# Kernel optimization log

Hardware: AMD Instinct MI355X
Metric: run time of the kernel (lower is better)

The kernel has to match this reference:

```python
import jax, jax.numpy as jnp
import numpy as np

B, S, HID = 1, 2048, 4096
NH, NKV = 32, 8
HD = HID // NH            # 128
GROUPS = NH // NKV        # 4
ROPE_THETA = 10000.0


def _rope_cos_sin(seq_len, head_dim, dtype=jnp.float32):
    inv_freq = 1.0 / (ROPE_THETA ** (jnp.arange(0, head_dim, 2, dtype=jnp.float32) / head_dim))
    t = jnp.arange(seq_len, dtype=jnp.float32)
    freqs = jnp.outer(t, inv_freq)                      # [S, HD/2]
    emb = jnp.concatenate([freqs, freqs], axis=-1)      # [S, HD]
    return jnp.cos(emb).astype(dtype), jnp.sin(emb).astype(dtype)


def _rotate_half(x):
    x1, x2 = jnp.split(x, 2, axis=-1)
    return jnp.concatenate([-x2, x1], axis=-1)


def _apply_rope(x, cos, sin):
    # x: [B, H, S, HD]; cos/sin: [S, HD] (position_ids = arange(S), no past)
    return x * cos[None, None] + _rotate_half(x) * sin[None, None]


def setup_inputs() -> dict:
    key = jax.random.key(0)
    k1, k2, k3, k4, k5 = jax.random.split(key, 5)
    return {
        "hidden_states": jax.random.normal(k1, (B, S, HID), jnp.float32),
        "Wq": jax.random.normal(k2, (NH * HD, HID), jnp.float32) * 0.02,
        "Wk": jax.random.normal(k3, (NKV * HD, HID), jnp.float32) * 0.02,
        "Wv": jax.random.normal(k4, (NKV * HD, HID), jnp.float32) * 0.02,
        "Wo": jax.random.normal(k5, (HID, NH * HD), jnp.float32) * 0.02,
    }


def reference(hidden_states, Wq, Wk, Wv, Wo):
    bsz, q_len, _ = hidden_states.shape
    # projections (nn.Linear: x @ W.T)
    q = (hidden_states @ Wq.T).reshape(bsz, q_len, NH, HD).transpose(0, 2, 1, 3)   # [B,NH,S,HD]
    k = (hidden_states @ Wk.T).reshape(bsz, q_len, NKV, HD).transpose(0, 2, 1, 3)  # [B,NKV,S,HD]
    v = (hidden_states @ Wv.T).reshape(bsz, q_len, NKV, HD).transpose(0, 2, 1, 3)

    cos, sin = _rope_cos_sin(q_len, HD, hidden_states.dtype)
    q = _apply_rope(q, cos, sin)
    k = _apply_rope(k, cos, sin)

    # GQA: repeat kv heads (repeat_kv / num_key_value_groups)
    k = jnp.repeat(k, GROUPS, axis=1)   # [B,NH,S,HD]
    v = jnp.repeat(v, GROUPS, axis=1)

    scale = 1.0 / jnp.sqrt(jnp.asarray(HD, hidden_states.dtype))
    logits = jnp.einsum('bhqd,bhkd->bhqk', q, k) * scale   # [B,NH,S,S]

    # prefill causal mask (phys_past_len = 0)
    causal = jnp.tril(jnp.ones((q_len, q_len), dtype=bool))
    logits = jnp.where(causal[None, None], logits, jnp.finfo(logits.dtype).min)

    attn = jax.nn.softmax(logits, axis=-1)
    out = jnp.einsum('bhqk,bhkd->bhqd', attn, v)            # [B,NH,S,HD]
    out = out.transpose(0, 2, 1, 3).reshape(bsz, q_len, NH * HD)
    return out @ Wo.T
```

## Files before the change

### kernel.cpp

```cpp
#include <hip/hip_runtime.h>

typedef __bf16 bf16;
typedef __bf16 bf16x2 __attribute__((ext_vector_type(2)));
typedef __bf16 bf16x4 __attribute__((ext_vector_type(4)));
typedef __bf16 bf16x8 __attribute__((ext_vector_type(8)));
typedef float f32x4 __attribute__((ext_vector_type(4)));

#define S_LEN 2048
#define HID_DIM 4096
#define NH 32
#define NKV 8
#define HD 128
#define QKV_N 6144
#define K_COL 4096
#define V_COL 5120
#define PADV 76

__global__ void cvt_all_kernel(const float* __restrict__ hs, const float* __restrict__ wq,
                               const float* __restrict__ wk, const float* __restrict__ wv,
                               const float* __restrict__ wo, bf16* __restrict__ hsb,
                               bf16* __restrict__ wqkvb, bf16* __restrict__ wob,
                               float* __restrict__ cost, float* __restrict__ sint) {
  long i = (long)blockIdx.x * blockDim.x + threadIdx.x;
  if (i >= 12582912) {
    int j = (int)(i - 12582912);
    int s = j >> 6, d = j & 63;
    float inv = expf(-0.14391156831212787f * (float)d);
    float ang = (float)s * inv;
    cost[j] = cosf(ang);
    sint[j] = sinf(ang);
    return;
  }
  const float* src; bf16* dst; long off; bool perm = false;
  if (i < 2097152)      { src = hs; dst = hsb;                          off = i; }
  else if (i < 6291456) { src = wq; dst = wqkvb;                        off = i - 2097152; perm = true; }
  else if (i < 7340032) { src = wk; dst = wqkvb + (long)4096 * 4096;    off = i - 6291456; perm = true; }
  else if (i < 8388608) { src = wv; dst = wqkvb + (long)5120 * 4096;    off = i - 7340032; }
  else                  { src = wo; dst = wob;                          off = i - 8388608; }
  float4 v = reinterpret_cast<const float4*>(src)[off];
  bf16x4 o;
  o[0] = (bf16)v.x; o[1] = (bf16)v.y; o[2] = (bf16)v.z; o[3] = (bf16)v.w;
  long doff = off;
  if (perm) {
    long r = off >> 10, c4 = off & 1023;
    long d = r & 127;
    long pd = ((d & 63) << 1) | (d >> 6);
    doff = (((r & ~127L) | pd) << 10) | c4;
  }
  reinterpret_cast<bf16x4*>(dst)[doff] = o;
}

#define STG8(buf, mat, kt, unit) {                                                       \
    const bf16* sp_ = (mat) ? Bp : Ap;                                                   \
    int row0_ = ((mat) ? n0 : m0) + (unit) * 64;                                         \
    int lb_ = (buf) * LBUF + (mat) * 16384 + (unit) * 4096;                              \
    int r_ = t >> 3, jl_ = t & 7, jg_ = jl_ ^ (r_ & 7);                                  \
    const bf16* src_ = sp_ + (long)(row0_ + r_) * K + (kt) * 64 + jg_ * 8;               \
    __builtin_amdgcn_global_load_lds((const __attribute__((address_space(1))) void*)src_,\
        (__attribute__((address_space(3))) void*)(L + lb_ + t * 8), 16, 0, 0); }

#define DSA2(buf, mh) {                                                                  \
    _Pragma("unroll") for (int ks_ = 0; ks_ < 2; ++ks_)                                  \
      _Pragma("unroll") for (int mf_ = 0; mf_ < 4; ++mf_) {                              \
        int R_ = wr * 128 + (mh) * 64 + mf_ * 16 + lm;                                   \
        aF[ks_][mf_] = *reinterpret_cast<const bf16x8*>(                                 \
            L + (buf) * LBUF + R_ * 64 + (((ks_ * 4 + lg) ^ (R_ & 7)) << 3));            \
      } }

#define DSBALL(buf) {                                                                    \
    _Pragma("unroll") for (int ks_ = 0; ks_ < 2; ++ks_)                                  \
      _Pragma("unroll") for (int nf_ = 0; nf_ < NB; ++nf_) {                             \
        int R_ = wc * (NB * 16) + nf_ * 16 + lm;                                         \
        bF[ks_][nf_] = *reinterpret_cast<const bf16x8*>(                                 \
            L + (buf) * LBUF + 16384 + R_ * 64 + (((ks_ * 4 + lg) ^ (R_ & 7)) << 3));    \
      } }

#define MM2(mh) {                                                                        \
    __builtin_amdgcn_s_setprio(1);                                                       \
    _Pragma("unroll") for (int mf_ = 0; mf_ < 4; ++mf_)                                  \
      _Pragma("unroll") for (int nf_ = 0; nf_ < NB; ++nf_)                               \
        _Pragma("unroll") for (int ks_ = 0; ks_ < 2; ++ks_)                              \
          acc[(mh) * 4 + mf_][nf_] = __builtin_amdgcn_mfma_f32_16x16x32_bf16(            \
              aF[ks_][mf_], bF[ks_][nf_], acc[(mh) * 4 + mf_][nf_], 0, 0, 0);            \
    __builtin_amdgcn_s_setprio(0); }

#define BAR() __builtin_amdgcn_s_barrier()
#define WVM(n) asm volatile("s_waitcnt vmcnt(%0)" :: "i"(n) : "memory")

template<int NB, bool ROPE, typename OutT>
__global__ __launch_bounds__(512, 1) void gemm4p_kernel(
    const bf16* __restrict__ Ap, const bf16* __restrict__ Bp, OutT* __restrict__ C,
    int M, int N, int K, const float* __restrict__ cost, const float* __restrict__ sint) {
  constexpr int LBUF = 16384 + NB * 4096;
  __shared__ __align__(16) bf16 L[2 * LBUF];

  int nwg = gridDim.x * gridDim.y;
  int bid = blockIdx.y * gridDim.x + blockIdx.x;
  int cpx = nwg >> 3;
  int swz = (bid & 7) * cpx + (bid >> 3);
  int bxs = swz % gridDim.x, bys = swz / gridDim.x;
  const int n0 = bxs * (NB * 64), m0 = bys * 256;

  const int t = threadIdx.x;
  const int lane = t & 63, w = t >> 6;
  const int wr = w >> 2, wc = w & 3;
  const int lg = lane >> 4, lm = lane & 15;
  const int NT = K >> 6;

  f32x4 acc[8][NB] = {};
  bf16x8 aF[2][4], bF[2][NB];

  STG8(0, 0, 0, 0); STG8(0, 0, 0, 1); STG8(0, 0, 0, 2); STG8(0, 0, 0, 3);
  STG8(0, 1, 0, 0); if (NB > 1) STG8(0, 1, 0, 1); if (NB > 2) STG8(0, 1, 0, 2);
  STG8(1, 1, 1, 0); if (NB > 1) STG8(1, 1, 1, 1); if (NB > 2) STG8(1, 1, 1, 2);
  WVM(NB);
  BAR();

  for (int I = 0; I < (NT >> 1); ++I) {
    const int tt = 2 * I;
    const bool pf = (I < (NT >> 1) - 1);
    DSA2(0, 0); DSBALL(0);
    STG8(1, 0, tt + 1, 0); STG8(1, 0, tt + 1, 1);
    STG8(1, 0, tt + 1, 2); STG8(1, 0, tt + 1, 3);
    BAR(); MM2(0); BAR();
    DSA2(0, 1);
    if (pf) { STG8(0, 1, tt + 2, 0); if (NB > 1) STG8(0, 1, tt + 2, 1);
              if (NB > 2) STG8(0, 1, tt + 2, 2); }
    BAR(); MM2(1);
    if (pf) WVM(NB); else WVM(0);
    BAR();
    DSA2(1, 0); DSBALL(1);
    if (pf) { STG8(0, 0, tt + 2, 0); STG8(0, 0, tt + 2, 1);
              STG8(0, 0, tt + 2, 2); STG8(0, 0, tt + 2, 3); }
    BAR(); MM2(0); BAR();
    DSA2(1, 1);
    if (pf) { STG8(1, 1, tt + 3, 0); if (NB > 1) STG8(1, 1, tt + 3, 1);
              if (NB > 2) STG8(1, 1, tt + 3, 2); }
    BAR(); MM2(1);
    if (pf) WVM(NB); else WVM(0);
    BAR();
  }

#pragma unroll
  for (int am = 0; am < 8; ++am) {
    int row = m0 + wr * 128 + am * 16 + lg * 4;
#pragma unroll
    for (int nf = 0; nf < NB; ++nf) {
      int col = n0 + wc * (NB * 16) + nf * 16 + lm;
      if (ROPE && col < V_COL) {
        int j = (col & 127) >> 1;
        bool odd = col & 1;
#pragma unroll
        for (int rr = 0; rr < 4; ++rr) {
          float x = acc[am][nf][rr];
          float xp = __shfl_xor(x, 1);
          int s = row + rr;
          float cv = cost[(s << 6) | j], sv = sint[(s << 6) | j];
          float y = odd ? (x * cv + xp * sv) : (x * cv - xp * sv);
          C[(long)s * N + col] = (bf16)y;
        }
      } else {
#pragma unroll
        for (int rr = 0; rr < 4; ++rr) {
          float v = acc[am][nf][rr];
          if constexpr (sizeof(OutT) == 4) C[(long)(row + rr) * N + col] = v;
          else                             C[(long)(row + rr) * N + col] = (bf16)v;
        }
      }
    }
  }
}

#define AK_BAR() { asm volatile("s_waitcnt vmcnt(2)" ::: "memory");                      \
                   __builtin_amdgcn_sched_barrier(0);                                    \
                   asm volatile("s_waitcnt lgkmcnt(0)" ::: "memory");                    \
                   __builtin_amdgcn_s_barrier(); }

#define AK_WRITEV(r0, r1, vtb) {                                                         \
    _Pragma("unroll") for (int e = 0; e < 8; ++e) {                                      \
      bf16x2 pk; pk[0] = r0[e]; pk[1] = r1[e];                                           \
      *reinterpret_cast<bf16x2*>(Vt[vtb] + (dchunk * 8 + e) * PADV + slot) = pk;         \
    } }

#define AK_ISSUEV(base, r0, r1) {                                                        \
    long rv_ = (long)(base) + kva; if (rv_ > 2046) rv_ = 2046;                           \
    const bf16* vs_ = vbase + rv_ * QKV_N + dchunk * 8;                                  \
    r0 = *reinterpret_cast<const bf16x8*>(vs_);                                          \
    r1 = *reinterpret_cast<const bf16x8*>(vs_ + QKV_N); }

#define AK_ISSUEK(base, buf) {                                                           \
    _Pragma("unroll") for (int i_ = 0; i_ < 2; ++i_) {                                   \
      int c_ = i_ * 512 + t;                                                             \
      int r_ = c_ >> 4, jl_ = c_ & 15, jg_ = jl_ ^ (r_ & 15);                            \
      long rk_ = (long)(base) + r_; if (rk_ > 2047) rk_ = 2047;                          \
      const bf16* src_ = kbase + rk_ * QKV_N + jg_ * 8;                                  \
      __builtin_amdgcn_global_load_lds((const __attribute__((address_space(1))) void*)src_,\
          (__attribute__((address_space(3))) void*)(Ks[buf] + c_ * 8), 16, 0, 0);        \
    } }

#define AK_STEP(stv, bufb) {                                                             \
    const int st_ = (stv);                                                               \
    const int kv0_ = st_ * 64;                                                           \
    if (kv0_ <= q0 + w * 16 + 15) {                                                      \
      f32x4 s[4];                                                                        \
      _Pragma("unroll") for (int cb = 0; cb < 4; ++cb) s[cb] = f32x4{0.f,0.f,0.f,0.f};   \
      __builtin_amdgcn_s_setprio(1);                                                     \
      _Pragma("unroll") for (int ks = 0; ks < 4; ++ks)                                   \
        _Pragma("unroll") for (int cb = 0; cb < 4; ++cb) {                               \
          bf16x8 kf = *reinterpret_cast<const bf16x8*>(                                  \
              Ks[bufb] + (cb * 16 + lm) * 128 + (((ks * 4 + lg) ^ lm) << 3));            \
          s[cb] = __builtin_amdgcn_mfma_f32_16x16x32_bf16(kf, qf[ks], s[cb], 0, 0, 0);   \
        }                                                                                \
      __builtin_amdgcn_s_setprio(0);                                                     \
      const float SC = 0.12751742f;                                                      \
      float sl[4][4];                                                                    \
      _Pragma("unroll") for (int cb = 0; cb < 4; ++cb)                                   \
        _Pragma("unroll") for (int r = 0; r < 4; ++r) {                                  \
          float v = s[cb][r] * SC;                                                       \
          if (st_ >= nst - 2 && (kv0_ + cb * 16 + lg * 4 + r) > qg) v = -1e30f;          \
          sl[cb][r] = v;                                                                 \
        }                                                                                \
      float tm = sl[0][0];                                                               \
      _Pragma("unroll") for (int cb = 0; cb < 4; ++cb)                                   \
        _Pragma("unroll") for (int r = 0; r < 4; ++r) tm = fmaxf(tm, sl[cb][r]);         \
      tm = fmaxf(tm, __shfl_xor(tm, 16));                                                \
      tm = fmaxf(tm, __shfl_xor(tm, 32));                                                \
      if (__any(tm > mrow + 8.f)) {                                                      \
        float mnew = fmaxf(mrow, tm);                                                    \
        float alpha = exp2f(mrow - mnew);                                                \
        mrow = mnew; lrow *= alpha;                                                      \
        float ar[4];                                                                     \
        _Pragma("unroll") for (int r = 0; r < 4; ++r)                                    \
          ar[r] = __shfl(alpha, (lane & 48) | (lg * 4 + r));                             \
        _Pragma("unroll") for (int i = 0; i < 8; ++i)                                    \
          _Pragma("unroll") for (int r = 0; r < 4; ++r) o[i][r] *= ar[r];                \
      }                                                                                  \
      float p[4][4]; float psum = 0.f;                                                   \
      _Pragma("unroll") for (int cb = 0; cb < 4; ++cb)                                   \
        _Pragma("unroll") for (int r = 0; r < 4; ++r) {                                  \
          p[cb][r] = exp2f(sl[cb][r] - mrow); psum += p[cb][r];                          \
        }                                                                                \
      psum += __shfl_xor(psum, 16);                                                      \
      psum += __shfl_xor(psum, 32);                                                      \
      lrow += psum;                                                                      \
      bf16x8 pa0, pa1;                                                                   \
      _Pragma("unroll") for (int r = 0; r < 4; ++r) {                                    \
        pa0[r] = (bf16)p[0][r]; pa0[4 + r] = (bf16)p[1][r];                              \
        pa1[r] = (bf16)p[2][r]; pa1[4 + r] = (bf16)p[3][r];                              \
      }                                                                                  \
      __builtin_amdgcn_s_setprio(1);                                                     \
      _Pragma("unroll") for (int db = 0; db < 8; ++db) {                                 \
        bf16x8 vf0 = *reinterpret_cast<const bf16x8*>(Vt[bufb] + (db*16+lm)*PADV + lg*8);\
        bf16x8 vf1 = *reinterpret_cast<const bf16x8*>(Vt[bufb] + (db*16+lm)*PADV + 32 + lg*8);\
        o[db] = __builtin_amdgcn_mfma_f32_16x16x32_bf16(pa0, vf0, o[db], 0, 0, 0);       \
        o[db] = __builtin_amdgcn_mfma_f32_16x16x32_bf16(pa1, vf1, o[db], 0, 0, 0);       \
      }                                                                                  \
      __builtin_amdgcn_s_setprio(0);                                                     \
    } }

__global__ __launch_bounds__(512, 4) void attn_kernel(const bf16* __restrict__ qkv,
                                                      bf16* __restrict__ out) {
  __shared__ __align__(16) bf16 Ks[2][64 * 128];
  __shared__ __align__(16) bf16 Vt[2][128 * PADV];

  const int bx = blockIdx.x;
  const int qt = (bx < 256) ? (15 - (bx >> 5)) : ((bx - 256) >> 5);
  const int h = bx & 31;
  const int kvh = h >> 2;
  const int q0 = qt * 128;
  const int t = threadIdx.x, lane = t & 63, w = t >> 6;
  const int lg = lane >> 4, lm = lane & 15;
  const int dchunk = t >> 5, kv2 = t & 31;
  const int kva = kv2 * 2;
  const int k5 = kva & 31;
  const int slot = ((kva >> 5) << 5) | (((k5 >> 2) & 3) << 3) | ((k5 >> 4) << 2) | (k5 & 3);
  const bf16* kbase = qkv + K_COL + kvh * HD;
  const bf16* vbase = qkv + V_COL + kvh * HD;

  const long qrow = q0 + w * 16 + lm;
  const int qg = q0 + w * 16 + lm;
  bf16x8 qf[4];
#pragma unroll
  for (int ks = 0; ks < 4; ++ks)
    qf[ks] = *reinterpret_cast<const bf16x8*>(qkv + qrow * QKV_N + h * HD + ks * 32 + lg * 8);

  f32x4 o[8];
#pragma unroll
  for (int i = 0; i < 8; ++i) o[i] = f32x4{0.f, 0.f, 0.f, 0.f};
  float mrow = -1e30f, lrow = 0.f;

  const int nst = 2 * qt + 2;
  bf16x8 va0, va1, vb0, vb1;

  AK_ISSUEK(0, 0);
  AK_ISSUEV(0, va0, va1);
  AK_WRITEV(va0, va1, 0);
  AK_ISSUEV(64, vb0, vb1);
  asm volatile("s_waitcnt lgkmcnt(0)" ::: "memory");
  __builtin_amdgcn_s_barrier();

  for (int I = 0; I < (nst >> 1); ++I) {
    const int s0 = 2 * I;
    AK_ISSUEK((s0 + 1) * 64, 1);
    AK_ISSUEV((s0 + 2) * 64, va0, va1);
    AK_WRITEV(vb0, vb1, 1);
    AK_STEP(s0, 0);
    AK_BAR();
    AK_ISSUEK((s0 + 2) * 64, 0);
    AK_ISSUEV((s0 + 3) * 64, vb0, vb1);
    AK_WRITEV(va0, va1, 0);
    AK_STEP(s0 + 1, 1);
    AK_BAR();
  }

  float invr[4];
#pragma unroll
  for (int r = 0; r < 4; ++r)
    invr[r] = 1.0f / __shfl(lrow, (lane & 48) | (lg * 4 + r));
#pragma unroll
  for (int r = 0; r < 4; ++r) {
    long row = q0 + w * 16 + lg * 4 + r;
#pragma unroll
    for (int db = 0; db < 8; ++db)
      out[row * HID_DIM + h * HD + db * 16 + lm] = (bf16)(o[db][r] * invr[r]);
  }
}

extern "C" void kernel_launch(void* const* d_in, const int* in_sizes, int n_in,
                              void* d_out, int out_size, void* d_ws, size_t ws_size,
                              hipStream_t stream) {
  const float* hs = (const float*)d_in[0];
  const float* Wq = (const float*)d_in[1];
  const float* Wk = (const float*)d_in[2];
  const float* Wv = (const float*)d_in[3];
  const float* Wo = (const float*)d_in[4];
  float* out = (float*)d_out;
  char* ws = (char*)d_ws;

  bf16*  hsb   = (bf16*)(ws);
  bf16*  wqkvb = (bf16*)(ws + 16777216);
  bf16*  wob   = (bf16*)(ws + 67108864);
  bf16*  qkv   = (bf16*)(ws + 100663296);
  bf16*  attn  = (bf16*)(ws + 125829120);
  float* cost  = (float*)(ws + 142606336);
  float* sint  = (float*)(ws + 143130624);

  cvt_all_kernel<<<49664, 256, 0, stream>>>(hs, Wq, Wk, Wv, Wo, hsb, wqkvb, wob, cost, sint);
  gemm4p_kernel<3, true, bf16><<<dim3(32, 8), 512, 0, stream>>>(hsb, wqkvb, qkv, 2048, 6144, 4096, cost, sint);
  attn_kernel<<<512, 512, 0, stream>>>(qkv, attn);
  gemm4p_kernel<2, false, float><<<dim3(32, 8), 512, 0, stream>>>(attn, wob, out, 2048, 4096, 4096, nullptr, nullptr);
}
```

Measured before the change: 297.5 us.

## Rework attention kernel to 32x32x16 MFMA with 4 waves of 32 query rows

The attention kernel switches from 16x16x32 MFMA tiles with 8 waves of 16 query rows to 32x32x16 MFMA tiles with 4 waves of 32 query rows each (256 threads per block). K/V staging loads are widened per thread to cover the tile with half the threads, and the Vt swizzle and softmax row-shuffle indexing are rewritten for the 32x32 accumulator layout. Separately, RoPE cos/sin tables are interleaved into a single float2 array so the QKV GEMM epilogue does one load instead of two. The larger MFMA tile aims for more compute per LDS fragment read, at the cost of higher register pressure per wave and fewer threads to hide latency.

```diff
diff --git a/kernel.cpp b/kernel.cpp
--- a/kernel.cpp
+++ b/kernel.cpp
@@ -5,6 +5,7 @@
 typedef __bf16 bf16x4 __attribute__((ext_vector_type(4)));
 typedef __bf16 bf16x8 __attribute__((ext_vector_type(8)));
 typedef float f32x4 __attribute__((ext_vector_type(4)));
+typedef float f32x16 __attribute__((ext_vector_type(16)));
 
 #define S_LEN 2048
 #define HID_DIM 4096
@@ -20,15 +21,14 @@
                                const float* __restrict__ wk, const float* __restrict__ wv,
                                const float* __restrict__ wo, bf16* __restrict__ hsb,
                                bf16* __restrict__ wqkvb, bf16* __restrict__ wob,
-                               float* __restrict__ cost, float* __restrict__ sint) {
+                               float2* __restrict__ csf) {
   long i = (long)blockIdx.x * blockDim.x + threadIdx.x;
   if (i >= 12582912) {
     int j = (int)(i - 12582912);
     int s = j >> 6, d = j & 63;
     float inv = expf(-0.14391156831212787f * (float)d);
     float ang = (float)s * inv;
-    cost[j] = cosf(ang);
-    sint[j] = sinf(ang);
+    csf[j] = make_float2(cosf(ang), sinf(ang));
     return;
   }
   const float* src; bf16* dst; long off; bool perm = false;
@@ -90,7 +90,7 @@
 template<int NB, bool ROPE, typename OutT>
 __global__ __launch_bounds__(512, 1) void gemm4p_kernel(
     const bf16* __restrict__ Ap, const bf16* __restrict__ Bp, OutT* __restrict__ C,
-    int M, int N, int K, const float* __restrict__ cost, const float* __restrict__ sint) {
+    int M, int N, int K, const float2* __restrict__ csf) {
   constexpr int LBUF = 16384 + NB * 4096;
   __shared__ __align__(16) bf16 L[2 * LBUF];
 
@@ -155,8 +155,8 @@
           float x = acc[am][nf][rr];
           float xp = __shfl_xor(x, 1);
           int s = row + rr;
-          float cv = cost[(s << 6) | j], sv = sint[(s << 6) | j];
-          float y = odd ? (x * cv + xp * sv) : (x * cv - xp * sv);
+          float2 cs = csf[(s << 6) | j];
+          float y = odd ? (x * cs.x + xp * cs.y) : (x * cs.x - xp * cs.y);
           C[(long)s * N + col] = (bf16)y;
         }
       } else {
@@ -171,26 +171,32 @@
   }
 }
 
-#define AK_BAR() { asm volatile("s_waitcnt vmcnt(2)" ::: "memory");                      \
+#define AK_BAR() { asm volatile("s_waitcnt vmcnt(4)" ::: "memory");                      \
                    __builtin_amdgcn_sched_barrier(0);                                    \
                    asm volatile("s_waitcnt lgkmcnt(0)" ::: "memory");                    \
                    __builtin_amdgcn_s_barrier(); }
 
-#define AK_WRITEV(r0, r1, vtb) {                                                         \
+#define AK_ISSUEV(base, ra0, ra1, rb0, rb1) {                                            \
+    long rv_ = (long)(base) + kva; if (rv_ > 2046) rv_ = 2046;                           \
+    const bf16* vs_ = vbase + rv_ * QKV_N + dchunk * 16;                                 \
+    ra0 = *reinterpret_cast<const bf16x8*>(vs_);                                         \
+    rb0 = *reinterpret_cast<const bf16x8*>(vs_ + 8);                                     \
+    ra1 = *reinterpret_cast<const bf16x8*>(vs_ + QKV_N);                                 \
+    rb1 = *reinterpret_cast<const bf16x8*>(vs_ + QKV_N + 8); }
+
+#define AK_WRITEV(ra0, ra1, rb0, rb1, vtb) {                                             \
     _Pragma("unroll") for (int e = 0; e < 8; ++e) {                                      \
-      bf16x2 pk; pk[0] = r0[e]; pk[1] = r1[e];                                           \
-      *reinterpret_cast<bf16x2*>(Vt[vtb] + (dchunk * 8 + e) * PADV + slot) = pk;         \
+      bf16x2 pk; pk[0] = ra0[e]; pk[1] = ra1[e];                                         \
+      *reinterpret_cast<bf16x2*>(Vt[vtb] + (dchunk * 16 + e) * PADV + slot) = pk;        \
+    }                                                                                    \
+    _Pragma("unroll") for (int e = 0; e < 8; ++e) {                                      \
+      bf16x2 pk; pk[0] = rb0[e]; pk[1] = rb1[e];                                         \
+      *reinterpret_cast<bf16x2*>(Vt[vtb] + (dchunk * 16 + 8 + e) * PADV + slot) = pk;    \
     } }
 
-#define AK_ISSUEV(base, r0, r1) {                                                        \
-    long rv_ = (long)(base) + kva; if (rv_ > 2046) rv_ = 2046;                           \
-    const bf16* vs_ = vbase + rv_ * QKV_N + dchunk * 8;                                  \
-    r0 = *reinterpret_cast<const bf16x8*>(vs_);                                          \
-    r1 = *reinterpret_cast<const bf16x8*>(vs_ + QKV_N); }
-
 #define AK_ISSUEK(base, buf) {                                                           \
-    _Pragma("unroll") for (int i_ = 0; i_ < 2; ++i_) {                                   \
-      int c_ = i_ * 512 + t;                                                             \
+    _Pragma("unroll") for (int i_ = 0; i_ < 4; ++i_) {                                   \
+      int c_ = i_ * 256 + t;                                                             \
       int r_ = c_ >> 4, jl_ = c_ & 15, jg_ = jl_ ^ (r_ & 15);                            \
       long rk_ = (long)(base) + r_; if (rk_ > 2047) rk_ = 2047;                          \
       const bf16* src_ = kbase + rk_ * QKV_N + jg_ * 8;                                  \
@@ -201,64 +207,63 @@
 #define AK_STEP(stv, bufb) {                                                             \
     const int st_ = (stv);                                                               \
     const int kv0_ = st_ * 64;                                                           \
-    if (kv0_ <= q0 + w * 16 + 15) {                                                      \
-      f32x4 s[4];                                                                        \
-      _Pragma("unroll") for (int cb = 0; cb < 4; ++cb) s[cb] = f32x4{0.f,0.f,0.f,0.f};   \
+    if (kv0_ <= q0 + w * 32 + 31) {                                                      \
+      f32x16 s0t, s1t;                                                                   \
+      _Pragma("unroll") for (int e = 0; e < 16; ++e) { s0t[e] = 0.f; s1t[e] = 0.f; }     \
       __builtin_amdgcn_s_setprio(1);                                                     \
-      _Pragma("unroll") for (int ks = 0; ks < 4; ++ks)                                   \
-        _Pragma("unroll") for (int cb = 0; cb < 4; ++cb) {                               \
-          bf16x8 kf = *reinterpret_cast<const bf16x8*>(                                  \
-              Ks[bufb] + (cb * 16 + lm) * 128 + (((ks * 4 + lg) ^ lm) << 3));            \
-          s[cb] = __builtin_amdgcn_mfma_f32_16x16x32_bf16(kf, qf[ks], s[cb], 0, 0, 0);   \
-        }                                                                                \
+      _Pragma("unroll") for (int c0 = 0; c0 < 8; ++c0) {                                 \
+        int swz_ = ((2 * c0 + hi) ^ (lane & 15)) << 3;                                   \
+        bf16x8 k0 = *reinterpret_cast<const bf16x8*>(Ks[bufb] + ql * 128 + swz_);        \
+        bf16x8 k1 = *reinterpret_cast<const bf16x8*>(Ks[bufb] + (32 + ql) * 128 + swz_); \
+        s0t = __builtin_amdgcn_mfma_f32_32x32x16_bf16(k0, qf[c0], s0t, 0, 0, 0);         \
+        s1t = __builtin_amdgcn_mfma_f32_32x32x16_bf16(k1, qf[c0], s1t, 0, 0, 0);         \
+      }                                                                                  \
       __builtin_amdgcn_s_setprio(0);                                                     \
       const float SC = 0.12751742f;                                                      \
-      float sl[4][4];                                                                    \
-      _Pragma("unroll") for (int cb = 0; cb < 4; ++cb)                                   \
-        _Pragma("unroll") for (int r = 0; r < 4; ++r) {                                  \
-          float v = s[cb][r] * SC;                                                       \
-          if (st_ >= nst - 2 && (kv0_ + cb * 16 + lg * 4 + r) > qg) v = -1e30f;          \
-          sl[cb][r] = v;                                                                 \
+      float sl[32];                                                                      \
+      _Pragma("unroll") for (int r = 0; r < 16; ++r) {                                   \
+        int kvr_ = (r & 3) + 8 * (r >> 2) + 4 * hi;                                      \
+        float v0 = s0t[r] * SC, v1 = s1t[r] * SC;                                        \
+        if (st_ >= nst - 2) {                                                            \
+          if (kv0_ + kvr_ > qg) v0 = -1e30f;                                             \
+          if (kv0_ + 32 + kvr_ > qg) v1 = -1e30f;                                        \
         }                                                                                \
-      float tm = sl[0][0];                                                               \
-      _Pragma("unroll") for (int cb = 0; cb < 4; ++cb)                                   \
-        _Pragma("unroll") for (int r = 0; r < 4; ++r) tm = fmaxf(tm, sl[cb][r]);         \
-      tm = fmaxf(tm, __shfl_xor(tm, 16));                                                \
+        sl[r] = v0; sl[16 + r] = v1;                                                     \
+      }                                                                                  \
+      float tm = sl[0];                                                                  \
+      _Pragma("unroll") for (int e = 1; e < 32; ++e) tm = fmaxf(tm, sl[e]);              \
       tm = fmaxf(tm, __shfl_xor(tm, 32));                                                \
       if (__any(tm > mrow + 8.f)) {                                                      \
         float mnew = fmaxf(mrow, tm);                                                    \
         float alpha = exp2f(mrow - mnew);                                                \
         mrow = mnew; lrow *= alpha;                                                      \
-        float ar[4];                                                                     \
-        _Pragma("unroll") for (int r = 0; r < 4; ++r)                                    \
-          ar[r] = __shfl(alpha, (lane & 48) | (lg * 4 + r));                             \
-        _Pragma("unroll") for (int i = 0; i < 8; ++i)                                    \
-          _Pragma("unroll") for (int r = 0; r < 4; ++r) o[i][r] *= ar[r];                \
+        float ar[16];                                                                    \
+        _Pragma("unroll") for (int r = 0; r < 16; ++r)                                   \
+          ar[r] = __shfl(alpha, (r & 3) + 8 * (r >> 2) + 4 * hi);                        \
+        _Pragma("unroll") for (int dt = 0; dt < 4; ++dt)                                 \
+          _Pragma("unroll") for (int r = 0; r < 16; ++r) o[dt][r] *= ar[r];              \
       }                                                                                  \
-      float p[4][4]; float psum = 0.f;                                                   \
-      _Pragma("unroll") for (int cb = 0; cb < 4; ++cb)                                   \
-        _Pragma("unroll") for (int r = 0; r < 4; ++r) {                                  \
-          p[cb][r] = exp2f(sl[cb][r] - mrow); psum += p[cb][r];                          \
-        }                                                                                \
-      psum += __shfl_xor(psum, 16);                                                      \
+      float pr[32]; float psum = 0.f;                                                    \
+      _Pragma("unroll") for (int e = 0; e < 32; ++e) {                                   \
+        pr[e] = exp2f(sl[e] - mrow); psum += pr[e];                                      \
+      }                                                                                  \
       psum += __shfl_xor(psum, 32);                                                      \
       lrow += psum;                                                                      \
-      bf16x8 pa0, pa1;                                                                   \
-      _Pragma("unroll") for (int r = 0; r < 4; ++r) {                                    \
-        pa0[r] = (bf16)p[0][r]; pa0[4 + r] = (bf16)p[1][r];                              \
-        pa1[r] = (bf16)p[2][r]; pa1[4 + r] = (bf16)p[3][r];                              \
-      }                                                                                  \
+      bf16x8 pa[4];                                                                      \
+      _Pragma("unroll") for (int pt = 0; pt < 4; ++pt)                                   \
+        _Pragma("unroll") for (int j = 0; j < 8; ++j)                                    \
+          pa[pt][j] = (bf16)pr[(pt >> 1) * 16 + j + 8 * (pt & 1)];                       \
       __builtin_amdgcn_s_setprio(1);                                                     \
-      _Pragma("unroll") for (int db = 0; db < 8; ++db) {                                 \
-        bf16x8 vf0 = *reinterpret_cast<const bf16x8*>(Vt[bufb] + (db*16+lm)*PADV + lg*8);\
-        bf16x8 vf1 = *reinterpret_cast<const bf16x8*>(Vt[bufb] + (db*16+lm)*PADV + 32 + lg*8);\
-        o[db] = __builtin_amdgcn_mfma_f32_16x16x32_bf16(pa0, vf0, o[db], 0, 0, 0);       \
-        o[db] = __builtin_amdgcn_mfma_f32_16x16x32_bf16(pa1, vf1, o[db], 0, 0, 0);       \
-      }                                                                                  \
+      _Pragma("unroll") for (int dt = 0; dt < 4; ++dt)                                   \
+        _Pragma("unroll") for (int pt = 0; pt < 4; ++pt) {                               \
+          bf16x8 vf = *reinterpret_cast<const bf16x8*>(                                  \
+              Vt[bufb] + (dt * 32 + ql) * PADV + pt * 16 + 8 * hi);                      \
+          o[dt] = __builtin_amdgcn_mfma_f32_32x32x16_bf16(pa[pt], vf, o[dt], 0, 0, 0);   \
+        }                                                                                \
       __builtin_amdgcn_s_setprio(0);                                                     \
     } }
 
-__global__ __launch_bounds__(512, 4) void attn_kernel(const bf16* __restrict__ qkv,
+__global__ __launch_bounds__(256, 2) void attn_kernel(const bf16* __restrict__ qkv,
                                                       bf16* __restrict__ out) {
   __shared__ __align__(16) bf16 Ks[2][64 * 128];
   __shared__ __align__(16) bf16 Vt[2][128 * PADV];
@@ -269,60 +274,59 @@
   const int kvh = h >> 2;
   const int q0 = qt * 128;
   const int t = threadIdx.x, lane = t & 63, w = t >> 6;
-  const int lg = lane >> 4, lm = lane & 15;
+  const int ql = lane & 31, hi = lane >> 5;
   const int dchunk = t >> 5, kv2 = t & 31;
   const int kva = kv2 * 2;
-  const int k5 = kva & 31;
-  const int slot = ((kva >> 5) << 5) | (((k5 >> 2) & 3) << 3) | ((k5 >> 4) << 2) | (k5 & 3);
+  const int slot = (kva & ~12) | ((kva & 8) >> 1) | ((kva & 4) << 1);
   const bf16* kbase = qkv + K_COL + kvh * HD;
   const bf16* vbase = qkv + V_COL + kvh * HD;
 
-  const long qrow = q0 + w * 16 + lm;
-  const int qg = q0 + w * 16 + lm;
-  bf16x8 qf[4];
-#pragma unroll
-  for (int ks = 0; ks < 4; ++ks)
-    qf[ks] = *reinterpret_cast<const bf16x8*>(qkv + qrow * QKV_N + h * HD + ks * 32 + lg * 8);
-
-  f32x4 o[8];
-#pragma unroll
-  for (int i = 0; i < 8; ++i) o[i] = f32x4{0.f, 0.f, 0.f, 0.f};
+  const long qrow = q0 + w * 32 + ql;
+  const int qg = q0 + w * 32 + ql;
+  bf16x8 qf[8];
+#pragma unroll
+  for (int c0 = 0; c0 < 8; ++c0)
+    qf[c0] = *reinterpret_cast<const bf16x8*>(qkv + qrow * QKV_N + h * HD + c0 * 16 + hi * 8);
+
+  f32x16 o[4];
+#pragma unroll
+  for (int dt = 0; dt < 4; ++dt)
+#pragma unroll
+    for (int e = 0; e < 16; ++e) o[dt][e] = 0.f;
   float mrow = -1e30f, lrow = 0.f;
 
   const int nst = 2 * qt + 2;
-  bf16x8 va0, va1, vb0, vb1;
+  bf16x8 va0, va1, va2, va3, vb0, vb1, vb2, vb3;
 
   AK_ISSUEK(0, 0);
-  AK_ISSUEV(0, va0, va1);
-  AK_WRITEV(va0, va1, 0);
-  AK_ISSUEV(64, vb0, vb1);
+  AK_ISSUEV(0, va0, va1, va2, va3);
+  AK_WRITEV(va0, va1, va2, va3, 0);
+  AK_ISSUEV(64, vb0, vb1, vb2, vb3);
   asm volatile("s_waitcnt lgkmcnt(0)" ::: "memory");
   __builtin_amdgcn_s_barrier();
 
   for (int I = 0; I < (nst >> 1); ++I) {
     const int s0 = 2 * I;
     AK_ISSUEK((s0 + 1) * 64, 1);
-    AK_ISSUEV((s0 + 2) * 64, va0, va1);
-    AK_WRITEV(vb0, vb1, 1);
+    AK_ISSUEV((s0 + 2) * 64, va0, va1, va2, va3);
+    AK_WRITEV(vb0, vb1, vb2, vb3, 1);
     AK_STEP(s0, 0);
     AK_BAR();
     AK_ISSUEK((s0 + 2) * 64, 0);
-    AK_ISSUEV((s0 + 3) * 64, vb0, vb1);
-    AK_WRITEV(va0, va1, 0);
+    AK_ISSUEV((s0 + 3) * 64, vb0, vb1, vb2, vb3);
+    AK_WRITEV(va0, va1, va2, va3, 0);
     AK_STEP(s0 + 1, 1);
     AK_BAR();
   }
 
-  float invr[4];
-#pragma unroll
-  for (int r = 0; r < 4; ++r)
-    invr[r] = 1.0f / __shfl(lrow, (lane & 48) | (lg * 4 + r));
-#pragma unroll
-  for (int r = 0; r < 4; ++r) {
-    long row = q0 + w * 16 + lg * 4 + r;
-#pragma unroll
-    for (int db = 0; db < 8; ++db)
-      out[row * HID_DIM + h * HD + db * 16 + lm] = (bf16)(o[db][r] * invr[r]);
+#pragma unroll
+  for (int r = 0; r < 16; ++r) {
+    int rowq = (r & 3) + 8 * (r >> 2) + 4 * hi;
+    float iv = 1.0f / __shfl(lrow, rowq);
+    long row = q0 + w * 32 + rowq;
+#pragma unroll
+    for (int dt = 0; dt < 4; ++dt)
+      out[row * HID_DIM + h * HD + dt * 32 + ql] = (bf16)(o[dt][r] * iv);
   }
 }
 
@@ -337,16 +341,15 @@
   float* out = (float*)d_out;
   char* ws = (char*)d_ws;
 
-  bf16*  hsb   = (bf16*)(ws);
-  bf16*  wqkvb = (bf16*)(ws + 16777216);
-  bf16*  wob   = (bf16*)(ws + 67108864);
-  bf16*  qkv   = (bf16*)(ws + 100663296);
-  bf16*  attn  = (bf16*)(ws + 125829120);
-  float* cost  = (float*)(ws + 142606336);
-  float* sint  = (float*)(ws + 143130624);
-
-  cvt_all_kernel<<<49664, 256, 0, stream>>>(hs, Wq, Wk, Wv, Wo, hsb, wqkvb, wob, cost, sint);
-  gemm4p_kernel<3, true, bf16><<<dim3(32, 8), 512, 0, stream>>>(hsb, wqkvb, qkv, 2048, 6144, 4096, cost, sint);
-  attn_kernel<<<512, 512, 0, stream>>>(qkv, attn);
-  gemm4p_kernel<2, false, float><<<dim3(32, 8), 512, 0, stream>>>(attn, wob, out, 2048, 4096, 4096, nullptr, nullptr);
+  bf16*   hsb   = (bf16*)(ws);
+  bf16*   wqkvb = (bf16*)(ws + 16777216);
+  bf16*   wob   = (bf16*)(ws + 67108864);
+  bf16*   qkv   = (bf16*)(ws + 100663296);
+  bf16*   attn  = (bf16*)(ws + 125829120);
+  float2* csf   = (float2*)(ws + 142606336);
+
+  cvt_all_kernel<<<49664, 256, 0, stream>>>(hs, Wq, Wk, Wv, Wo, hsb, wqkvb, wob, csf);
+  gemm4p_kernel<3, true, bf16><<<dim3(32, 8), 512, 0, stream>>>(hsb, wqkvb, qkv, 2048, 6144, 4096, csf);
+  attn_kernel<<<512, 256, 0, stream>>>(qkv, attn);
+  gemm4p_kernel<2, false, float><<<dim3(32, 8), 512, 0, stream>>>(attn, wob, out, 2048, 4096, 4096, nullptr);
 }
```

Measured after the change: 313.1 us. 1.05x slower.
